# Optimization experiments

Hardware: AMD Instinct MI355X
Metric: run time of the kernel (lower is better)

## Reference

```python
import jax, jax.numpy as jnp
import numpy as np

# dims: T timesteps, B batch, IN input, OUT output, H controller hidden,
# N mem slots, C mem cell size, R read heads
T, B, IN, OUT, H, N, C, R = 512, 64, 256, 256, 512, 2048, 64, 4
EPS = 1e-8


def setup_inputs() -> dict:
    key = jax.random.key(0)
    ks = jax.random.split(key, 12)
    s = 0.02
    d_in = IN + C * R  # controller sees x_t concat flattened read vectors
    return {
        "xs": jax.random.normal(ks[0], (T, B, IN), jnp.float32),
        "W_ih": jax.random.normal(ks[1], (d_in, 4 * H), jnp.float32) * s,
        "W_hh": jax.random.normal(ks[2], (H, 4 * H), jnp.float32) * s,
        "b_lstm": jnp.zeros((4 * H,), jnp.float32),
        "W_out": jax.random.normal(ks[3], (H, OUT), jnp.float32) * s,
        "b_out": jnp.zeros((OUT,), jnp.float32),
        "W_key": jax.random.normal(ks[4], (H, C), jnp.float32) * s,
        "b_key": jnp.zeros((C,), jnp.float32),
        "W_beta": jax.random.normal(ks[5], (H, 1), jnp.float32) * s,
        "b_beta": jnp.zeros((1,), jnp.float32),
        "W_gen": jax.random.normal(ks[6], (H, C), jnp.float32) * s,
        "b_gen": jnp.zeros((C,), jnp.float32),
    }


def reference(xs, W_ih, W_hh, b_lstm, W_out, b_out, W_key, b_key,
              W_beta, b_beta, W_gen, b_gen):
    Bx = xs.shape[1]
    mem0 = jnp.zeros((Bx, N, C), xs.dtype)
    h0 = jnp.zeros((Bx, H), xs.dtype)
    c0 = jnp.zeros((Bx, H), xs.dtype)
    rv0 = jnp.zeros((Bx, C, R), xs.dtype)
    sl0 = jnp.zeros((), xs.dtype)

    def step(carry, x_t):
        h, c, mem, rv, sl = carry
        inp = jnp.concatenate([x_t, rv.reshape(Bx, -1)], axis=-1)
        gates = inp @ W_ih + h @ W_hh + b_lstm
        i_g, f_g, g_g, o_g = jnp.split(gates, 4, axis=-1)
        c = jax.nn.sigmoid(f_g) * c + jax.nn.sigmoid(i_g) * jnp.tanh(g_g)
        h = jax.nn.sigmoid(o_g) * jnp.tanh(c)
        pre_out = h @ W_out + b_out                    # (B, OUT)
        key = h @ W_key + b_key                        # (B, C)
        beta = jax.nn.softplus(h @ W_beta + b_beta)    # (B, 1)
        gen = h @ W_gen + b_gen                        # (B, C)
        # cosine similarity between each memory slot and the key
        num = jnp.einsum('bnc,bc->bn', mem, key)
        den = (jnp.maximum(jnp.linalg.norm(mem, axis=-1), EPS)
               * jnp.maximum(jnp.linalg.norm(key, axis=-1, keepdims=True), EPS))
        sim = num / den                                # (B, N)
        w = jax.nn.softmax(beta * sim, axis=-1)        # (B, N)
        # supervised (teacher) loss for this step
        sl = sl + jnp.mean((key - gen) ** 2)
        # additive content write: rank-1 update
        mem = mem + w[:, :, None] * key[:, None, :]
        # read: weights are the write weights repeated over read heads,
        # so all heads read the same vector -> compute once and broadcast
        r = jnp.einsum('bn,bnc->bc', w, mem)           # (B, C)
        rv = jnp.broadcast_to(r[:, :, None], (Bx, C, R))
        return (h, c, mem, rv, sl), pre_out

    (h, c, mem, rv, sup_loss), y_all = jax.lax.scan(
        step, (h0, c0, mem0, rv0, sl0), xs)
    return y_all, sup_loss
```

## Files before the change

kernel.cpp:

```cpp
#include <hip/hip_runtime.h>
#include <hip/hip_fp16.h>

#define EPSF 1e-8f
#define SCOPE_AGT __HIP_MEMORY_SCOPE_AGENT


typedef _Float16 h2_t __attribute__((ext_vector_type(2)));

struct P4 {
  const unsigned* W2h;
  const _Float16* Wkg;
  const _Float16* Wy;
  const float* b_lstm;
  const float* b_out;
  const float* b_key;
  const float* W_beta;
  const float* b_beta;
  const float* b_gen;
  const float* xs;
  float* hbuf;
  float* keyP;
  float* genP;
  float* yP;
  float* betaP;
  float* AccP;
  float* ZP;
  float* S2P;
  unsigned* ctr;
  float* out;
};

__device__ __forceinline__ float sigm(float x) { return 1.f / (1.f + __expf(-x)); }
__device__ __forceinline__ float aload(const float* p) {
  return __hip_atomic_load(p, __ATOMIC_RELAXED, SCOPE_AGT);
}
__device__ __forceinline__ void astore(float* p, float v) {
  __hip_atomic_store(p, v, __ATOMIC_RELAXED, SCOPE_AGT);
}

__global__ void __launch_bounds__(1024, 4) dnc_b4(P4 P) {
  const int tid   = threadIdx.x;
  const int bid   = blockIdx.x;
  const int chunk = (bid >> 1) & 3;
  const int b     = ((bid >> 3) << 1) | (bid & 1);
  const int lane  = tid & 63;
  const int wv    = tid >> 6;
  const int sgrp  = lane >> 4;
  const int c4    = lane & 15;

  __shared__ float s_inp[832];
  __shared__ float s_gates[512];
  __shared__ float s_c[128];
  __shared__ float s_part[4096];
  __shared__ float s_e[512];
  __shared__ float s_key[64], s_kprev[64], s_genv[64];
  __shared__ float s_wred[32];
  __shared__ float s_scal[4];

  unsigned* ctr = P.ctr + b * 32;

  float4 mreg[8];
  float  sden[8];
#pragma unroll
  for (int i = 0; i < 8; ++i) mreg[i] = make_float4(0.f, 0.f, 0.f, 0.f);

  for (int i = 256 + tid; i < 832; i += 1024) s_inp[i] = 0.f;
  if (tid < 128) s_c[tid] = 0.f;
  if (tid < 512) s_e[tid] = 0.f;
  if (tid < 64)  s_kprev[tid] = 0.f;
  float lossacc = 0.f;
  __syncthreads();

  const int q  = tid >> 7;
  const int cg = tid & 127;
  const unsigned* wbase = P.W2h + (size_t)chunk * 212992 + (cg << 2);

  for (int t = 0; t < 512; ++t) {
    if (tid < 128)
      ((float2*)s_inp)[tid] = ((const float2*)P.xs)[((size_t)t * 64 + b) * 128 + tid];
    __syncthreads();

    float4 acc = make_float4(0.f, 0.f, 0.f, 0.f);
    {
      const unsigned* wp = wbase + (size_t)(q * 48) * 512;
      const float* ip = s_inp + q * 96;
#pragma unroll 4
      for (int r = 0; r < 48; ++r) {
        const uint4 w = *(const uint4*)(wp + (size_t)r * 512);
        const float2 v = *(const float2*)(ip + r * 2);
        const __half2* h2 = (const __half2*)&w;
        const float2 f0 = __half22float2(h2[0]), f1 = __half22float2(h2[1]);
        const float2 f2 = __half22float2(h2[2]), f3 = __half22float2(h2[3]);
        acc.x = fmaf(v.x, f0.x, fmaf(v.y, f0.y, acc.x));
        acc.y = fmaf(v.x, f1.x, fmaf(v.y, f1.y, acc.y));
        acc.z = fmaf(v.x, f2.x, fmaf(v.y, f2.y, acc.z));
        acc.w = fmaf(v.x, f3.x, fmaf(v.y, f3.y, acc.w));
      }
    }

    if (t > 0) {
      if (tid == 0) {
        while (__hip_atomic_load(ctr, __ATOMIC_RELAXED, SCOPE_AGT) < 8u * (unsigned)t)
          __builtin_amdgcn_s_sleep(1);
      }
      __syncthreads();
      float a0 = 0.f, a1 = 0.f, a2 = 0.f, a3 = 0.f;
      if (tid < 64) {
        const float* ap = P.AccP + b * 256 + tid;
        a0 = aload(ap); a1 = aload(ap + 64); a2 = aload(ap + 128); a3 = aload(ap + 192);
      } else if (tid == 64) {
        const float* zp = P.ZP + b * 4;
        const float* sp = P.S2P + b * 4;
        const float Z  = aload(zp) + aload(zp + 1) + aload(zp + 2) + aload(zp + 3);
        const float S2 = aload(sp) + aload(sp + 1) + aload(sp + 2) + aload(sp + 3);
        s_scal[0] = 1.f / Z;  s_scal[1] = S2;
      }
      __syncthreads();
      if (tid < 64) {
        const float iZ = s_scal[0];
        s_inp[768 + tid] = iZ * ((a0 + a1 + a2 + a3) + s_scal[1] * iZ * s_kprev[tid]);
      }
      __syncthreads();
    } else {
      if (tid == 64) { s_scal[0] = 0.f; s_scal[1] = 0.f; }
      __syncthreads();
    }

    {
      const unsigned* wp = wbase + (size_t)(384 + q * 4) * 512;
      const float* ip = s_inp + 768 + q * 8;
#pragma unroll
      for (int r = 0; r < 4; ++r) {
        const uint4 w = *(const uint4*)(wp + (size_t)r * 512);
        const float2 v = *(const float2*)(ip + r * 2);
        const __half2* h2 = (const __half2*)&w;
        const float2 f0 = __half22float2(h2[0]), f1 = __half22float2(h2[1]);
        const float2 f2 = __half22float2(h2[2]), f3 = __half22float2(h2[3]);
        acc.x = fmaf(v.x, f0.x, fmaf(v.y, f0.y, acc.x));
        acc.y = fmaf(v.x, f1.x, fmaf(v.y, f1.y, acc.y));
        acc.z = fmaf(v.x, f2.x, fmaf(v.y, f2.y, acc.z));
        acc.w = fmaf(v.x, f3.x, fmaf(v.y, f3.y, acc.w));
      }
    }
    *(float4*)&s_part[(q << 9) + (cg << 2)] = acc;
    __syncthreads();

    if (tid < 512) {
      s_gates[tid] = s_part[tid]        + s_part[512 + tid]  + s_part[1024 + tid] + s_part[1536 + tid]
                   + s_part[2048 + tid] + s_part[2560 + tid] + s_part[3072 + tid] + s_part[3584 + tid];
    }
    __syncthreads();
    if (tid < 128) {
      const int jl = tid, cb = chunk * 128 + jl;
      const float gi = s_gates[jl * 4 + 0] + P.b_lstm[cb];
      const float gf = s_gates[jl * 4 + 1] + P.b_lstm[512 + cb];
      const float gg = s_gates[jl * 4 + 2] + P.b_lstm[1024 + cb];
      const float go = s_gates[jl * 4 + 3] + P.b_lstm[1536 + cb];
      const float cn = sigm(gf) * s_c[jl] + sigm(gi) * tanhf(gg);
      s_c[jl] = cn;
      const float hn = sigm(go) * tanhf(cn);
      s_inp[256 + cb] = hn;
      astore(P.hbuf + b * 512 + cb, hn);
    }
    __syncthreads();

    {
      const float* h = s_inp + 256 + chunk * 128;
      {
        const int isg = tid >> 9, rg = (tid >> 6) & 7, c = tid & 63;
        const _Float16* wp2 = P.Wkg + (size_t)(chunk * 128 + rg * 16) * 128 + isg * 64 + c;
        const float* hh = h + rg * 16;
        float a2 = 0.f;
#pragma unroll
        for (int r2 = 0; r2 < 16; ++r2) a2 = fmaf(hh[r2], (float)wp2[(size_t)r2 * 128], a2);
        s_part[tid] = a2;
      }
      {
        const int rg = tid >> 8, col = tid & 255;
        const _Float16* wp2 = P.Wy + (size_t)(chunk * 128 + rg * 32) * 256 + col;
        const float* hh = h + rg * 32;
        float a2 = 0.f;
#pragma unroll 8
        for (int r2 = 0; r2 < 32; ++r2) a2 = fmaf(hh[r2], (float)wp2[(size_t)r2 * 256], a2);
        s_part[1024 + (rg << 8) + col] = a2;
      }
      {
        float pb = (tid < 128) ? h[tid] * P.W_beta[chunk * 128 + tid] : 0.f;
#pragma unroll
        for (int off = 32; off; off >>= 1) pb += __shfl_down(pb, off);
        if (tid < 128 && lane == 0) s_wred[wv] = pb;
      }
    }
    __syncthreads();
    if (tid < 64) {
      float v = 0.f;
#pragma unroll
      for (int k = 0; k < 8; ++k) v += s_part[k * 64 + tid];
      astore(P.keyP + (b * 4 + chunk) * 64 + tid, v);
    } else if (tid < 128) {
      const int c = tid - 64;
      float v = 0.f;
#pragma unroll
      for (int k = 0; k < 8; ++k) v += s_part[512 + k * 64 + c];
      astore(P.genP + (b * 4 + chunk) * 64 + c, v);
    } else if (tid < 384) {
      const int col = tid - 128;
      astore(P.yP + (b * 4 + chunk) * 256 + col,
             s_part[1024 + col] + s_part[1280 + col] + s_part[1536 + col] + s_part[1792 + col]);
    } else if (tid == 384) {
      astore(P.betaP + b * 4 + chunk, s_wred[0] + s_wred[1]);
    }
    __syncthreads();
    if (tid == 0) __hip_atomic_fetch_add(ctr, 1u, __ATOMIC_RELEASE, SCOPE_AGT);

    {
      const float invZp = s_scal[0];
      const float4 kp4 = ((const float4*)s_kprev)[c4];
      const int nbase = (wv * 4 + sgrp) * 8;
#pragma unroll
      for (int it = 0; it < 8; ++it) {
        float4 m4 = mreg[it];
        const float wpv = s_e[nbase + it] * invZp;
        m4.x = fmaf(wpv, kp4.x, m4.x); m4.y = fmaf(wpv, kp4.y, m4.y);
        m4.z = fmaf(wpv, kp4.z, m4.z); m4.w = fmaf(wpv, kp4.w, m4.w);
        float ssq = m4.x * m4.x + m4.y * m4.y + m4.z * m4.z + m4.w * m4.w;
#pragma unroll
        for (int off = 1; off < 16; off <<= 1) ssq += __shfl_xor(ssq, off);
        sden[it] = fmaxf(sqrtf(ssq), EPSF);
        mreg[it] = m4;
      }
    }

    if (tid == 0) {
      while (__hip_atomic_load(ctr, __ATOMIC_RELAXED, SCOPE_AGT) < 8u * (unsigned)t + 4u)
        __builtin_amdgcn_s_sleep(1);
    }
    __syncthreads();
    if (tid < 64) {
      const float* kp = P.keyP + b * 256 + tid;
      s_key[tid] = aload(kp) + aload(kp + 64) + aload(kp + 128) + aload(kp + 192) + P.b_key[tid];
    } else if (tid < 128) {
      const int c = tid - 64;
      const float* gp = P.genP + b * 256 + c;
      s_genv[c] = aload(gp) + aload(gp + 64) + aload(gp + 128) + aload(gp + 192) + P.b_gen[c];
    } else if (tid < 192) {
      const int col = tid - 128, oc = chunk * 64 + col;
      const float* yp = P.yP + b * 1024 + oc;
      P.out[((size_t)t * 64 + b) * 256 + oc] =
          aload(yp) + aload(yp + 256) + aload(yp + 512) + aload(yp + 768) + P.b_out[oc];
    } else if (tid == 192) {
      const float* bp = P.betaP + b * 4;
      const float s = aload(bp) + aload(bp + 1) + aload(bp + 2) + aload(bp + 3) + P.b_beta[0];
      s_scal[2] = (s > 20.f) ? s : log1pf(__expf(s));
    } else if (tid >= 256 && tid < 640) {
      const int i = tid - 256;
      const int pc = i >> 7;
      const int pcc = pc + (pc >= chunk ? 1 : 0);
      const int jl = i & 127;
      s_inp[256 + pcc * 128 + jl] = aload(P.hbuf + b * 512 + pcc * 128 + jl);
    }
    __syncthreads();
    if (wv == 0) {
      const float kv = s_key[lane];
      float sq = kv * kv;
#pragma unroll
      for (int off = 32; off; off >>= 1) sq += __shfl_down(sq, off);
      if (lane == 0) s_scal[3] = fmaxf(sqrtf(sq), EPSF);
    } else if (wv == 1 && chunk == 0) {
      const float d = s_key[lane] - s_genv[lane];
      float ds = d * d;
#pragma unroll
      for (int off = 32; off; off >>= 1) ds += __shfl_down(ds, off);
      if (lane == 0) lossacc += ds;
    }
    __syncthreads();

    {
      const float beta = s_scal[2], kn = s_scal[3];
      const float4 kk = ((const float4*)s_key)[c4];
      float Zp = 0.f, S2p = 0.f;
      float4 acc4 = make_float4(0.f, 0.f, 0.f, 0.f);
      const int nbase = (wv * 4 + sgrp) * 8;
#pragma unroll
      for (int it = 0; it < 8; ++it) {
        const float4 m4 = mreg[it];
        float num = m4.x * kk.x + m4.y * kk.y + m4.z * kk.z + m4.w * kk.w;
#pragma unroll
        for (int off = 1; off < 16; off <<= 1) num += __shfl_xor(num, off);
        const float e = __expf(beta * (num / (sden[it] * kn)));
        if (c4 == 0) { s_e[nbase + it] = e; Zp += e; S2p += e * e; }
        acc4.x = fmaf(e, m4.x, acc4.x); acc4.y = fmaf(e, m4.y, acc4.y);
        acc4.z = fmaf(e, m4.z, acc4.z); acc4.w = fmaf(e, m4.w, acc4.w);
      }
#pragma unroll
      for (int off = 32; off; off >>= 1) { Zp += __shfl_down(Zp, off); S2p += __shfl_down(S2p, off); }
      if (lane == 0) { s_wred[wv] = Zp; s_wred[16 + wv] = S2p; }
#pragma unroll
      for (int off = 16; off < 64; off <<= 1) {
        acc4.x += __shfl_down(acc4.x, off); acc4.y += __shfl_down(acc4.y, off);
        acc4.z += __shfl_down(acc4.z, off); acc4.w += __shfl_down(acc4.w, off);
      }
      if (lane < 16) ((float4*)s_part)[wv * 16 + lane] = acc4;
    }
    __syncthreads();
    if (tid < 64) {
      float a = 0.f;
#pragma unroll
      for (int w = 0; w < 16; ++w) a += s_part[w * 64 + tid];
      astore(P.AccP + (b * 4 + chunk) * 64 + tid, a);
      s_kprev[tid] = s_key[tid];
    } else if (tid == 64) {
      float Z = 0.f, S2 = 0.f;
#pragma unroll
      for (int k = 0; k < 16; ++k) { Z += s_wred[k]; S2 += s_wred[16 + k]; }
      astore(P.ZP + b * 4 + chunk, Z);
      astore(P.S2P + b * 4 + chunk, S2);
    }
    __syncthreads();
    if (tid == 0) __hip_atomic_fetch_add(ctr, 1u, __ATOMIC_RELEASE, SCOPE_AGT);
  }

  if (chunk == 0 && tid == 64) atomicAdd(P.out + 8388608, lossacc * (1.f / 4096.f));
}

__global__ void build_w2h(const float* __restrict__ W_ih, const float* __restrict__ W_hh,
                          unsigned* __restrict__ W2h) {
  const int id = blockIdx.x * 256 + threadIdx.x;
  if (id >= 851968) return;
  const int chunk = id / 212992;
  const int rem   = id % 212992;
  const int rp    = rem >> 9;
  const int cc    = rem & 511;
  const int jl = cc >> 2, g = cc & 3;
  const int col = g * 512 + chunk * 128 + jl;
  float v[2];
#pragma unroll
  for (int k = 0; k < 2; ++k) {
    const int row = rp * 2 + k;
    if (row < 256)      v[k] = W_ih[(size_t)row * 2048 + col];
    else if (row < 768) v[k] = W_hh[(size_t)(row - 256) * 2048 + col];
    else {
      const float* p0 = W_ih + (size_t)(256 + (row - 768) * 4) * 2048 + col;
      v[k] = p0[0] + p0[2048] + p0[4096] + p0[6144];
    }
  }
  const __half2 h2v = __floats2half2_rn(v[0], v[1]);
  W2h[id] = *(const unsigned*)&h2v;
}

__global__ void build_wkg(const float* __restrict__ W_key, const float* __restrict__ W_gen,
                          _Float16* __restrict__ Wkg) {
  const int id = blockIdx.x * 256 + threadIdx.x;
  if (id >= 65536) return;
  const int row = id >> 7, cl = id & 127;
  const float v = (cl < 64) ? W_key[(size_t)row * 64 + cl] : W_gen[(size_t)row * 64 + cl - 64];
  Wkg[id] = (_Float16)v;
}

__global__ void build_wy(const float* __restrict__ W_out, _Float16* __restrict__ Wy) {
  const int id = blockIdx.x * 256 + threadIdx.x;
  if (id >= 131072) return;
  Wy[id] = (_Float16)W_out[id];
}

extern "C" void kernel_launch(void* const* d_in, const int* in_sizes, int n_in,
                              void* d_out, int out_size, void* d_ws, size_t ws_size,
                              hipStream_t stream) {
  const float* xs     = (const float*)d_in[0];
  const float* W_ih   = (const float*)d_in[1];
  const float* W_hh   = (const float*)d_in[2];
  const float* b_lstm = (const float*)d_in[3];
  const float* W_out  = (const float*)d_in[4];
  const float* b_out  = (const float*)d_in[5];
  const float* W_key  = (const float*)d_in[6];
  const float* b_key  = (const float*)d_in[7];
  const float* W_beta = (const float*)d_in[8];
  const float* b_beta = (const float*)d_in[9];
  const float* W_gen  = (const float*)d_in[10];
  const float* b_gen  = (const float*)d_in[11];
  float* out = (float*)d_out;

  float* ws = (float*)d_ws;
  unsigned* W2h = (unsigned*)ws;
  _Float16* Wkg = (_Float16*)(ws + 851968);
  _Float16* Wy  = (_Float16*)(ws + 884736);
  float* hbuf  = ws     + 950272;
  float* keyP  = hbuf   + 32768;
  float* genP  = keyP   + 16384;
  float* yP    = genP   + 16384;
  float* betaP = yP     + 65536;
  float* AccP  = betaP  + 256;
  float* ZP    = AccP   + 16384;
  float* S2P   = ZP     + 256;
  unsigned* ctr = (unsigned*)(S2P + 256);

  hipMemsetAsync(ctr, 0, 2048 * sizeof(unsigned), stream);
  hipMemsetAsync(out + 8388608, 0, sizeof(float), stream);

  build_w2h<<<dim3(3328), dim3(256), 0, stream>>>(W_ih, W_hh, W2h);
  build_wkg<<<dim3(256), dim3(256), 0, stream>>>(W_key, W_gen, Wkg);
  build_wy<<<dim3(512),  dim3(256), 0, stream>>>(W_out, Wy);

  P4 prm;
  prm.W2h = W2h; prm.Wkg = Wkg; prm.Wy = Wy;
  prm.b_lstm = b_lstm; prm.b_out = b_out; prm.b_key = b_key;
  prm.W_beta = W_beta; prm.b_beta = b_beta; prm.b_gen = b_gen;
  prm.xs = xs;
  prm.hbuf = hbuf; prm.keyP = keyP; prm.genP = genP; prm.yP = yP; prm.betaP = betaP;
  prm.AccP = AccP; prm.ZP = ZP; prm.S2P = S2P;
  prm.ctr = ctr;  prm.out = out;

  void* kargs[] = { &prm };
  hipLaunchCooperativeKernel(reinterpret_cast<void*>(&dnc_b4),
                             dim3(256), dim3(1024), kargs, 0, stream);
}
```

Before: 13.21 ms.

## Process two batch rows per block and use packed fp16 dot2 for matvecs

Each block now handles two batch elements instead of one, halving the grid to 128 blocks, so every weight load from the fp16 LSTM, key/gen and output matrices is reused for two rows. The matvec inputs are stored as fp16 in shared memory and accumulated with the fdot2 builtin on pair-packed weight layouts, and the key/gen/output weights are repacked as half2 pairs. Memory state for both rows is kept in registers, which doubles register and shared-memory pressure per block and halves parallelism across the device. Feeding h, x and the read vector as fp16 also lowers input precision.

Measured after the change: 25.31 ms. 91.7% more time.

```diff
diff --git a/kernel.cpp b/kernel.cpp
--- a/kernel.cpp
+++ b/kernel.cpp
@@ -7,10 +7,10 @@
 
 typedef _Float16 h2_t __attribute__((ext_vector_type(2)));
 
-struct P4 {
+struct P11 {
   const unsigned* W2h;
-  const _Float16* Wkg;
-  const _Float16* Wy;
+  const unsigned* Wkg2;
+  const unsigned* Wy2;
   const float* b_lstm;
   const float* b_out;
   const float* b_key;
@@ -37,37 +37,58 @@
 __device__ __forceinline__ void astore(float* p, float v) {
   __hip_atomic_store(p, v, __ATOMIC_RELAXED, SCOPE_AGT);
 }
-
-__global__ void __launch_bounds__(1024, 4) dnc_b4(P4 P) {
+__device__ __forceinline__ h2_t u2h(unsigned u) {
+  union { unsigned u; h2_t h; } x; x.u = u; return x.h;
+}
+
+#if defined(__has_builtin)
+#if __has_builtin(__builtin_amdgcn_fdot2)
+#define HAVE_FDOT2 1
+#endif
+#endif
+
+__device__ __forceinline__ float dot2acc(h2_t a, h2_t b, float c) {
+#ifdef HAVE_FDOT2
+  return __builtin_amdgcn_fdot2(a, b, c, false);
+#else
+  return fmaf((float)a.x, (float)b.x, fmaf((float)a.y, (float)b.y, c));
+#endif
+}
+
+__global__ void __launch_bounds__(1024, 4) dnc_b11(P11 P) {
   const int tid   = threadIdx.x;
   const int bid   = blockIdx.x;
   const int chunk = (bid >> 1) & 3;
-  const int b     = ((bid >> 3) << 1) | (bid & 1);
+  const int bp    = ((bid >> 3) << 1) | (bid & 1);
+  const int b0    = bp * 2;
   const int lane  = tid & 63;
   const int wv    = tid >> 6;
   const int sgrp  = lane >> 4;
   const int c4    = lane & 15;
 
-  __shared__ float s_inp[832];
-  __shared__ float s_gates[512];
-  __shared__ float s_c[128];
-  __shared__ float s_part[4096];
-  __shared__ float s_e[512];
-  __shared__ float s_key[64], s_kprev[64], s_genv[64];
-  __shared__ float s_wred[32];
-  __shared__ float s_scal[4];
-
-  unsigned* ctr = P.ctr + b * 32;
-
-  float4 mreg[8];
-  float  sden[8];
-#pragma unroll
-  for (int i = 0; i < 8; ++i) mreg[i] = make_float4(0.f, 0.f, 0.f, 0.f);
-
-  for (int i = 256 + tid; i < 832; i += 1024) s_inp[i] = 0.f;
-  if (tid < 128) s_c[tid] = 0.f;
-  if (tid < 512) s_e[tid] = 0.f;
-  if (tid < 64)  s_kprev[tid] = 0.f;
+  __shared__ _Float16 s_ih[2][832];
+  __shared__ float s_gates[2][512];
+  __shared__ float s_c[2][128];
+  __shared__ float s_part[8192];
+  __shared__ float s_e[2][512];
+  __shared__ float s_den[2][512];
+  __shared__ float s_key[2][64], s_kprev[2][64], s_genv[2][64];
+  __shared__ float s_wrZA[16], s_wrSA[16], s_wrZB[16], s_wrSB[16];
+  __shared__ float s_bred[2][2];
+  __shared__ float s_scal[2][4];
+
+  unsigned* ctr = P.ctr + bp * 32;
+
+  float4 mreg[2][8];
+#pragma unroll
+  for (int bb = 0; bb < 2; ++bb)
+#pragma unroll
+    for (int i = 0; i < 8; ++i) mreg[bb][i] = make_float4(0.f, 0.f, 0.f, 0.f);
+
+  for (int i = tid; i < 2 * 832; i += 1024) ((_Float16*)s_ih)[i] = (_Float16)0.f;
+  if (tid < 512) { s_e[0][tid] = 0.f; s_e[1][tid] = 0.f; }
+  if (tid < 128) { s_c[0][tid] = 0.f; s_c[1][tid] = 0.f; s_kprev[tid >> 6][tid & 63] = 0.f; }
+  if (tid < 8) s_scal[tid >> 2][tid & 3] = 0.f;
   float lossacc = 0.f;
   __syncthreads();
 
@@ -76,25 +97,29 @@
   const unsigned* wbase = P.W2h + (size_t)chunk * 212992 + (cg << 2);
 
   for (int t = 0; t < 512; ++t) {
-    if (tid < 128)
-      ((float2*)s_inp)[tid] = ((const float2*)P.xs)[((size_t)t * 64 + b) * 128 + tid];
-    __syncthreads();
-
-    float4 acc = make_float4(0.f, 0.f, 0.f, 0.f);
+    if (tid < 256) {
+      const int bb = tid >> 7, i = tid & 127;
+      const float2 xv = ((const float2*)P.xs)[((size_t)t * 64 + b0 + bb) * 128 + i];
+      h2_t hv; hv.x = (_Float16)xv.x; hv.y = (_Float16)xv.y;
+      *(h2_t*)&s_ih[bb][i * 2] = hv;
+    }
+    __syncthreads();
+
+    float4 accA = make_float4(0.f, 0.f, 0.f, 0.f);
+    float4 accB = make_float4(0.f, 0.f, 0.f, 0.f);
     {
       const unsigned* wp = wbase + (size_t)(q * 48) * 512;
-      const float* ip = s_inp + q * 96;
+      const _Float16* iA = &s_ih[0][q * 96];
+      const _Float16* iB = &s_ih[1][q * 96];
 #pragma unroll 4
       for (int r = 0; r < 48; ++r) {
         const uint4 w = *(const uint4*)(wp + (size_t)r * 512);
-        const float2 v = *(const float2*)(ip + r * 2);
-        const __half2* h2 = (const __half2*)&w;
-        const float2 f0 = __half22float2(h2[0]), f1 = __half22float2(h2[1]);
-        const float2 f2 = __half22float2(h2[2]), f3 = __half22float2(h2[3]);
-        acc.x = fmaf(v.x, f0.x, fmaf(v.y, f0.y, acc.x));
-        acc.y = fmaf(v.x, f1.x, fmaf(v.y, f1.y, acc.y));
-        acc.z = fmaf(v.x, f2.x, fmaf(v.y, f2.y, acc.z));
-        acc.w = fmaf(v.x, f3.x, fmaf(v.y, f3.y, acc.w));
+        const h2_t vA = *(const h2_t*)(iA + r * 2);
+        const h2_t vB = *(const h2_t*)(iB + r * 2);
+        accA.x = dot2acc(u2h(w.x), vA, accA.x); accB.x = dot2acc(u2h(w.x), vB, accB.x);
+        accA.y = dot2acc(u2h(w.y), vA, accA.y); accB.y = dot2acc(u2h(w.y), vB, accB.y);
+        accA.z = dot2acc(u2h(w.z), vA, accA.z); accB.z = dot2acc(u2h(w.z), vB, accB.z);
+        accA.w = dot2acc(u2h(w.w), vA, accA.w); accB.w = dot2acc(u2h(w.w), vB, accB.w);
       }
     }
 
@@ -105,129 +130,156 @@
       }
       __syncthreads();
       float a0 = 0.f, a1 = 0.f, a2 = 0.f, a3 = 0.f;
-      if (tid < 64) {
-        const float* ap = P.AccP + b * 256 + tid;
+      if (tid < 128) {
+        const int bb = tid >> 6, c = tid & 63;
+        const float* ap = P.AccP + (b0 + bb) * 256 + c;
         a0 = aload(ap); a1 = aload(ap + 64); a2 = aload(ap + 128); a3 = aload(ap + 192);
-      } else if (tid == 64) {
-        const float* zp = P.ZP + b * 4;
-        const float* sp = P.S2P + b * 4;
+      } else if (tid < 130) {
+        const int bb = tid - 128;
+        const float* zp = P.ZP + (b0 + bb) * 4;
+        const float* sp = P.S2P + (b0 + bb) * 4;
         const float Z  = aload(zp) + aload(zp + 1) + aload(zp + 2) + aload(zp + 3);
         const float S2 = aload(sp) + aload(sp + 1) + aload(sp + 2) + aload(sp + 3);
-        s_scal[0] = 1.f / Z;  s_scal[1] = S2;
+        s_scal[bb][0] = 1.f / Z;  s_scal[bb][1] = S2;
       }
       __syncthreads();
-      if (tid < 64) {
-        const float iZ = s_scal[0];
-        s_inp[768 + tid] = iZ * ((a0 + a1 + a2 + a3) + s_scal[1] * iZ * s_kprev[tid]);
+      if (tid < 128) {
+        const int bb = tid >> 6, c = tid & 63;
+        const float iZ = s_scal[bb][0];
+        const float r = iZ * ((a0 + a1 + a2 + a3) + s_scal[bb][1] * iZ * s_kprev[bb][c]);
+        s_ih[bb][768 + c] = (_Float16)r;
       }
       __syncthreads();
     } else {
-      if (tid == 64) { s_scal[0] = 0.f; s_scal[1] = 0.f; }
       __syncthreads();
     }
 
     {
       const unsigned* wp = wbase + (size_t)(384 + q * 4) * 512;
-      const float* ip = s_inp + 768 + q * 8;
+      const _Float16* iA = &s_ih[0][768 + q * 8];
+      const _Float16* iB = &s_ih[1][768 + q * 8];
 #pragma unroll
       for (int r = 0; r < 4; ++r) {
         const uint4 w = *(const uint4*)(wp + (size_t)r * 512);
-        const float2 v = *(const float2*)(ip + r * 2);
-        const __half2* h2 = (const __half2*)&w;
-        const float2 f0 = __half22float2(h2[0]), f1 = __half22float2(h2[1]);
-        const float2 f2 = __half22float2(h2[2]), f3 = __half22float2(h2[3]);
-        acc.x = fmaf(v.x, f0.x, fmaf(v.y, f0.y, acc.x));
-        acc.y = fmaf(v.x, f1.x, fmaf(v.y, f1.y, acc.y));
-        acc.z = fmaf(v.x, f2.x, fmaf(v.y, f2.y, acc.z));
-        acc.w = fmaf(v.x, f3.x, fmaf(v.y, f3.y, acc.w));
-      }
-    }
-    *(float4*)&s_part[(q << 9) + (cg << 2)] = acc;
-    __syncthreads();
-
-    if (tid < 512) {
-      s_gates[tid] = s_part[tid]        + s_part[512 + tid]  + s_part[1024 + tid] + s_part[1536 + tid]
-                   + s_part[2048 + tid] + s_part[2560 + tid] + s_part[3072 + tid] + s_part[3584 + tid];
-    }
-    __syncthreads();
-    if (tid < 128) {
-      const int jl = tid, cb = chunk * 128 + jl;
-      const float gi = s_gates[jl * 4 + 0] + P.b_lstm[cb];
-      const float gf = s_gates[jl * 4 + 1] + P.b_lstm[512 + cb];
-      const float gg = s_gates[jl * 4 + 2] + P.b_lstm[1024 + cb];
-      const float go = s_gates[jl * 4 + 3] + P.b_lstm[1536 + cb];
-      const float cn = sigm(gf) * s_c[jl] + sigm(gi) * tanhf(gg);
-      s_c[jl] = cn;
+        const h2_t vA = *(const h2_t*)(iA + r * 2);
+        const h2_t vB = *(const h2_t*)(iB + r * 2);
+        accA.x = dot2acc(u2h(w.x), vA, accA.x); accB.x = dot2acc(u2h(w.x), vB, accB.x);
+        accA.y = dot2acc(u2h(w.y), vA, accA.y); accB.y = dot2acc(u2h(w.y), vB, accB.y);
+        accA.z = dot2acc(u2h(w.z), vA, accA.z); accB.z = dot2acc(u2h(w.z), vB, accB.z);
+        accA.w = dot2acc(u2h(w.w), vA, accA.w); accB.w = dot2acc(u2h(w.w), vB, accB.w);
+      }
+    }
+    *(float4*)&s_part[(q << 9) + (cg << 2)]        = accA;
+    *(float4*)&s_part[4096 + (q << 9) + (cg << 2)] = accB;
+    __syncthreads();
+
+    {
+      const int bb = tid >> 9, col = tid & 511, off = bb * 4096;
+      float g = 0.f;
+#pragma unroll
+      for (int k = 0; k < 8; ++k) g += s_part[off + (k << 9) + col];
+      s_gates[bb][col] = g;
+    }
+    __syncthreads();
+
+    if (tid < 256) {
+      const int bb = tid >> 7, jl = tid & 127, cb = chunk * 128 + jl;
+      const float gi = s_gates[bb][jl * 4 + 0] + P.b_lstm[cb];
+      const float gf = s_gates[bb][jl * 4 + 1] + P.b_lstm[512 + cb];
+      const float gg = s_gates[bb][jl * 4 + 2] + P.b_lstm[1024 + cb];
+      const float go = s_gates[bb][jl * 4 + 3] + P.b_lstm[1536 + cb];
+      const float cn = sigm(gf) * s_c[bb][jl] + sigm(gi) * tanhf(gg);
+      s_c[bb][jl] = cn;
       const float hn = sigm(go) * tanhf(cn);
-      s_inp[256 + cb] = hn;
-      astore(P.hbuf + b * 512 + cb, hn);
-    }
-    __syncthreads();
-
-    {
-      const float* h = s_inp + 256 + chunk * 128;
+      s_ih[bb][256 + cb] = (_Float16)hn;
+      astore(P.hbuf + (b0 + bb) * 512 + cb, hn);
+    }
+    __syncthreads();
+
+    {
       {
         const int isg = tid >> 9, rg = (tid >> 6) & 7, c = tid & 63;
-        const _Float16* wp2 = P.Wkg + (size_t)(chunk * 128 + rg * 16) * 128 + isg * 64 + c;
-        const float* hh = h + rg * 16;
-        float a2 = 0.f;
-#pragma unroll
-        for (int r2 = 0; r2 < 16; ++r2) a2 = fmaf(hh[r2], (float)wp2[(size_t)r2 * 128], a2);
-        s_part[tid] = a2;
+#pragma unroll
+        for (int bb = 0; bb < 2; ++bb) {
+          float a = 0.f;
+#pragma unroll
+          for (int k = 0; k < 8; ++k) {
+            const unsigned w = P.Wkg2[(size_t)(chunk * 64 + rg * 8 + k) * 128 + isg * 64 + c];
+            const h2_t v = *(const h2_t*)&s_ih[bb][256 + chunk * 128 + rg * 16 + 2 * k];
+            a = dot2acc(u2h(w), v, a);
+          }
+          s_part[bb * 2048 + rg * 128 + isg * 64 + c] = a;
+        }
       }
       {
         const int rg = tid >> 8, col = tid & 255;
-        const _Float16* wp2 = P.Wy + (size_t)(chunk * 128 + rg * 32) * 256 + col;
-        const float* hh = h + rg * 32;
-        float a2 = 0.f;
-#pragma unroll 8
-        for (int r2 = 0; r2 < 32; ++r2) a2 = fmaf(hh[r2], (float)wp2[(size_t)r2 * 256], a2);
-        s_part[1024 + (rg << 8) + col] = a2;
+#pragma unroll
+        for (int bb = 0; bb < 2; ++bb) {
+          float a = 0.f;
+#pragma unroll
+          for (int k = 0; k < 16; ++k) {
+            const unsigned w = P.Wy2[(size_t)(chunk * 64 + rg * 16 + k) * 256 + col];
+            const h2_t v = *(const h2_t*)&s_ih[bb][256 + chunk * 128 + rg * 32 + 2 * k];
+            a = dot2acc(u2h(w), v, a);
+          }
+          s_part[bb * 2048 + 1024 + (rg << 8) + col] = a;
+        }
       }
       {
-        float pb = (tid < 128) ? h[tid] * P.W_beta[chunk * 128 + tid] : 0.f;
-#pragma unroll
-        for (int off = 32; off; off >>= 1) pb += __shfl_down(pb, off);
-        if (tid < 128 && lane == 0) s_wred[wv] = pb;
-      }
-    }
-    __syncthreads();
-    if (tid < 64) {
-      float v = 0.f;
-#pragma unroll
-      for (int k = 0; k < 8; ++k) v += s_part[k * 64 + tid];
-      astore(P.keyP + (b * 4 + chunk) * 64 + tid, v);
-    } else if (tid < 128) {
-      const int c = tid - 64;
-      float v = 0.f;
-#pragma unroll
-      for (int k = 0; k < 8; ++k) v += s_part[512 + k * 64 + c];
-      astore(P.genP + (b * 4 + chunk) * 64 + c, v);
-    } else if (tid < 384) {
-      const int col = tid - 128;
-      astore(P.yP + (b * 4 + chunk) * 256 + col,
-             s_part[1024 + col] + s_part[1280 + col] + s_part[1536 + col] + s_part[1792 + col]);
-    } else if (tid == 384) {
-      astore(P.betaP + b * 4 + chunk, s_wred[0] + s_wred[1]);
+        if (tid < 128 || (tid >= 512 && tid < 640)) {
+          const int bb = tid >> 9, i = tid & 127;
+          const float hv = (float)s_ih[bb][256 + chunk * 128 + i];
+          float pb = hv * P.W_beta[chunk * 128 + i];
+#pragma unroll
+          for (int off = 32; off; off >>= 1) pb += __shfl_down(pb, off);
+          if (lane == 0) s_bred[bb][wv & 1] = pb;
+        }
+      }
+    }
+    __syncthreads();
+    {
+      const int bb = tid >> 9, t2 = tid & 511, off = bb * 2048;
+      if (t2 < 64) {
+        float v = 0.f;
+#pragma unroll
+        for (int k = 0; k < 8; ++k) v += s_part[off + k * 128 + t2];
+        astore(P.keyP + ((b0 + bb) * 4 + chunk) * 64 + t2, v);
+      } else if (t2 < 128) {
+        const int c = t2 - 64;
+        float v = 0.f;
+#pragma unroll
+        for (int k = 0; k < 8; ++k) v += s_part[off + k * 128 + 64 + c];
+        astore(P.genP + ((b0 + bb) * 4 + chunk) * 64 + c, v);
+      } else if (t2 < 384) {
+        const int col = t2 - 128;
+        astore(P.yP + ((b0 + bb) * 4 + chunk) * 256 + col,
+               s_part[off + 1024 + col] + s_part[off + 1280 + col]
+             + s_part[off + 1536 + col] + s_part[off + 1792 + col]);
+      } else if (t2 == 384) {
+        astore(P.betaP + (b0 + bb) * 4 + chunk, s_bred[bb][0] + s_bred[bb][1]);
+      }
     }
     __syncthreads();
     if (tid == 0) __hip_atomic_fetch_add(ctr, 1u, __ATOMIC_RELEASE, SCOPE_AGT);
 
     {
-      const float invZp = s_scal[0];
-      const float4 kp4 = ((const float4*)s_kprev)[c4];
       const int nbase = (wv * 4 + sgrp) * 8;
 #pragma unroll
-      for (int it = 0; it < 8; ++it) {
-        float4 m4 = mreg[it];
-        const float wpv = s_e[nbase + it] * invZp;
-        m4.x = fmaf(wpv, kp4.x, m4.x); m4.y = fmaf(wpv, kp4.y, m4.y);
-        m4.z = fmaf(wpv, kp4.z, m4.z); m4.w = fmaf(wpv, kp4.w, m4.w);
-        float ssq = m4.x * m4.x + m4.y * m4.y + m4.z * m4.z + m4.w * m4.w;
-#pragma unroll
-        for (int off = 1; off < 16; off <<= 1) ssq += __shfl_xor(ssq, off);
-        sden[it] = fmaxf(sqrtf(ssq), EPSF);
-        mreg[it] = m4;
+      for (int bb = 0; bb < 2; ++bb) {
+        const float invZp = s_scal[bb][0];
+        const float4 kp4 = ((const float4*)s_kprev[bb])[c4];
+#pragma unroll
+        for (int it = 0; it < 8; ++it) {
+          float4 m4 = mreg[bb][it];
+          const float wpv = s_e[bb][nbase + it] * invZp;
+          m4.x = fmaf(wpv, kp4.x, m4.x); m4.y = fmaf(wpv, kp4.y, m4.y);
+          m4.z = fmaf(wpv, kp4.z, m4.z); m4.w = fmaf(wpv, kp4.w, m4.w);
+          float ssq = m4.x * m4.x + m4.y * m4.y + m4.z * m4.z + m4.w * m4.w;
+#pragma unroll
+          for (int off = 1; off < 16; off <<= 1) ssq += __shfl_xor(ssq, off);
+          if (c4 == 0) s_den[bb][nbase + it] = fmaxf(sqrtf(ssq), EPSF);
+          mreg[bb][it] = m4;
+        }
       }
     }
 
@@ -236,38 +288,48 @@
         __builtin_amdgcn_s_sleep(1);
     }
     __syncthreads();
-    if (tid < 64) {
-      const float* kp = P.keyP + b * 256 + tid;
-      s_key[tid] = aload(kp) + aload(kp + 64) + aload(kp + 128) + aload(kp + 192) + P.b_key[tid];
-    } else if (tid < 128) {
-      const int c = tid - 64;
-      const float* gp = P.genP + b * 256 + c;
-      s_genv[c] = aload(gp) + aload(gp + 64) + aload(gp + 128) + aload(gp + 192) + P.b_gen[c];
-    } else if (tid < 192) {
-      const int col = tid - 128, oc = chunk * 64 + col;
-      const float* yp = P.yP + b * 1024 + oc;
-      P.out[((size_t)t * 64 + b) * 256 + oc] =
-          aload(yp) + aload(yp + 256) + aload(yp + 512) + aload(yp + 768) + P.b_out[oc];
-    } else if (tid == 192) {
-      const float* bp = P.betaP + b * 4;
-      const float s = aload(bp) + aload(bp + 1) + aload(bp + 2) + aload(bp + 3) + P.b_beta[0];
-      s_scal[2] = (s > 20.f) ? s : log1pf(__expf(s));
-    } else if (tid >= 256 && tid < 640) {
-      const int i = tid - 256;
+    if (tid < 768) {
+      const int bb = (tid >= 384) ? 1 : 0;
+      const int i = tid - bb * 384;
       const int pc = i >> 7;
       const int pcc = pc + (pc >= chunk ? 1 : 0);
       const int jl = i & 127;
-      s_inp[256 + pcc * 128 + jl] = aload(P.hbuf + b * 512 + pcc * 128 + jl);
-    }
-    __syncthreads();
-    if (wv == 0) {
-      const float kv = s_key[lane];
+      const float hv = aload(P.hbuf + (b0 + bb) * 512 + pcc * 128 + jl);
+      s_ih[bb][256 + pcc * 128 + jl] = (_Float16)hv;
+    }
+    {
+      const int bb = tid >> 8;
+      const int t2 = tid & 255;
+      if (tid < 512) {
+        if (t2 < 64) {
+          const float* kp = P.keyP + (b0 + bb) * 256 + t2;
+          s_key[bb][t2] = aload(kp) + aload(kp + 64) + aload(kp + 128) + aload(kp + 192) + P.b_key[t2];
+        } else if (t2 < 128) {
+          const int c = t2 - 64;
+          const float* gp = P.genP + (b0 + bb) * 256 + c;
+          s_genv[bb][c] = aload(gp) + aload(gp + 64) + aload(gp + 128) + aload(gp + 192) + P.b_gen[c];
+        } else if (t2 < 192) {
+          const int col = t2 - 128, oc = chunk * 64 + col;
+          const float* yp = P.yP + (b0 + bb) * 1024 + oc;
+          P.out[((size_t)t * 64 + b0 + bb) * 256 + oc] =
+              aload(yp) + aload(yp + 256) + aload(yp + 512) + aload(yp + 768) + P.b_out[oc];
+        } else if (t2 == 192) {
+          const float* bpt = P.betaP + (b0 + bb) * 4;
+          const float s = aload(bpt) + aload(bpt + 1) + aload(bpt + 2) + aload(bpt + 3) + P.b_beta[0];
+          s_scal[bb][2] = (s > 20.f) ? s : log1pf(__expf(s));
+        }
+      }
+    }
+    __syncthreads();
+    if (wv < 2) {
+      const float kv = s_key[wv][lane];
       float sq = kv * kv;
 #pragma unroll
       for (int off = 32; off; off >>= 1) sq += __shfl_down(sq, off);
-      if (lane == 0) s_scal[3] = fmaxf(sqrtf(sq), EPSF);
-    } else if (wv == 1 && chunk == 0) {
-      const float d = s_key[lane] - s_genv[lane];
+      if (lane == 0) s_scal[wv][3] = fmaxf(sqrtf(sq), EPSF);
+    } else if ((wv == 2 || wv == 3) && chunk == 0) {
+      const int bb = wv - 2;
+      const float d = s_key[bb][lane] - s_genv[bb][lane];
       float ds = d * d;
 #pragma unroll
       for (int off = 32; off; off >>= 1) ds += __shfl_down(ds, off);
@@ -276,51 +338,88 @@
     __syncthreads();
 
     {
-      const float beta = s_scal[2], kn = s_scal[3];
-      const float4 kk = ((const float4*)s_key)[c4];
-      float Zp = 0.f, S2p = 0.f;
-      float4 acc4 = make_float4(0.f, 0.f, 0.f, 0.f);
       const int nbase = (wv * 4 + sgrp) * 8;
+      const float betaA = s_scal[0][2], knA = s_scal[0][3];
+      const float betaB = s_scal[1][2], knB = s_scal[1][3];
+      const float4 kkA = ((const float4*)s_key[0])[c4];
+      const float4 kkB = ((const float4*)s_key[1])[c4];
+      float ZpA = 0.f, S2pA = 0.f, ZpB = 0.f, S2pB = 0.f;
+      float4 acA = make_float4(0.f, 0.f, 0.f, 0.f);
+      float4 acB = make_float4(0.f, 0.f, 0.f, 0.f);
 #pragma unroll
       for (int it = 0; it < 8; ++it) {
-        const float4 m4 = mreg[it];
-        float num = m4.x * kk.x + m4.y * kk.y + m4.z * kk.z + m4.w * kk.w;
-#pragma unroll
-        for (int off = 1; off < 16; off <<= 1) num += __shfl_xor(num, off);
-        const float e = __expf(beta * (num / (sden[it] * kn)));
-        if (c4 == 0) { s_e[nbase + it] = e; Zp += e; S2p += e * e; }
-        acc4.x = fmaf(e, m4.x, acc4.x); acc4.y = fmaf(e, m4.y, acc4.y);
-        acc4.z = fmaf(e, m4.z, acc4.z); acc4.w = fmaf(e, m4.w, acc4.w);
-      }
-#pragma unroll
-      for (int off = 32; off; off >>= 1) { Zp += __shfl_down(Zp, off); S2p += __shfl_down(S2p, off); }
-      if (lane == 0) { s_wred[wv] = Zp; s_wred[16 + wv] = S2p; }
+        {
+          const float4 m4 = mreg[0][it];
+          float num = m4.x * kkA.x + m4.y * kkA.y + m4.z * kkA.z + m4.w * kkA.w;
+#pragma unroll
+          for (int off = 1; off < 16; off <<= 1) num += __shfl_xor(num, off);
+          const float e = __expf(betaA * (num / (s_den[0][nbase + it] * knA)));
+          if (c4 == 0) { s_e[0][nbase + it] = e; ZpA += e; S2pA += e * e; }
+          acA.x = fmaf(e, m4.x, acA.x); acA.y = fmaf(e, m4.y, acA.y);
+          acA.z = fmaf(e, m4.z, acA.z); acA.w = fmaf(e, m4.w, acA.w);
+        }
+        {
+          const float4 m4 = mreg[1][it];
+          float num = m4.x * kkB.x + m4.y * kkB.y + m4.z * kkB.z + m4.w * kkB.w;
+#pragma unroll
+          for (int off = 1; off < 16; off <<= 1) num += __shfl_xor(num, off);
+          const float e = __expf(betaB * (num / (s_den[1][nbase + it] * knB)));
+          if (c4 == 0) { s_e[1][nbase + it] = e; ZpB += e; S2pB += e * e; }
+          acB.x = fmaf(e, m4.x, acB.x); acB.y = fmaf(e, m4.y, acB.y);
+          acB.z = fmaf(e, m4.z, acB.z); acB.w = fmaf(e, m4.w, acB.w);
+        }
+      }
+#pragma unroll
+      for (int off = 32; off; off >>= 1) {
+        ZpA += __shfl_down(ZpA, off); S2pA += __shfl_down(S2pA, off);
+        ZpB += __shfl_down(ZpB, off); S2pB += __shfl_down(S2pB, off);
+      }
+      if (lane == 0) { s_wrZA[wv] = ZpA; s_wrSA[wv] = S2pA; s_wrZB[wv] = ZpB; s_wrSB[wv] = S2pB; }
 #pragma unroll
       for (int off = 16; off < 64; off <<= 1) {
-        acc4.x += __shfl_down(acc4.x, off); acc4.y += __shfl_down(acc4.y, off);
-        acc4.z += __shfl_down(acc4.z, off); acc4.w += __shfl_down(acc4.w, off);
-      }
-      if (lane < 16) ((float4*)s_part)[wv * 16 + lane] = acc4;
+        acA.x += __shfl_down(acA.x, off); acA.y += __shfl_down(acA.y, off);
+        acA.z += __shfl_down(acA.z, off); acA.w += __shfl_down(acA.w, off);
+        acB.x += __shfl_down(acB.x, off); acB.y += __shfl_down(acB.y, off);
+        acB.z += __shfl_down(acB.z, off); acB.w += __shfl_down(acB.w, off);
+      }
+      if (lane < 16) {
+        ((float4*)s_part)[wv * 16 + lane]       = acA;
+        ((float4*)s_part)[256 + wv * 16 + lane] = acB;
+      }
     }
     __syncthreads();
     if (tid < 64) {
       float a = 0.f;
 #pragma unroll
       for (int w = 0; w < 16; ++w) a += s_part[w * 64 + tid];
-      astore(P.AccP + (b * 4 + chunk) * 64 + tid, a);
-      s_kprev[tid] = s_key[tid];
+      astore(P.AccP + (b0 * 4 + chunk) * 64 + tid, a);
+      s_kprev[0][tid] = s_key[0][tid];
     } else if (tid == 64) {
       float Z = 0.f, S2 = 0.f;
 #pragma unroll
-      for (int k = 0; k < 16; ++k) { Z += s_wred[k]; S2 += s_wred[16 + k]; }
-      astore(P.ZP + b * 4 + chunk, Z);
-      astore(P.S2P + b * 4 + chunk, S2);
+      for (int k = 0; k < 16; ++k) { Z += s_wrZA[k]; S2 += s_wrSA[k]; }
+      astore(P.ZP + b0 * 4 + chunk, Z);
+      astore(P.S2P + b0 * 4 + chunk, S2);
+    } else if (tid >= 128 && tid < 192) {
+      const int c = tid - 128;
+      float a = 0.f;
+#pragma unroll
+      for (int w = 0; w < 16; ++w) a += s_part[1024 + w * 64 + c];
+      astore(P.AccP + ((b0 + 1) * 4 + chunk) * 64 + c, a);
+      s_kprev[1][c] = s_key[1][c];
+    } else if (tid == 192) {
+      float Z = 0.f, S2 = 0.f;
+#pragma unroll
+      for (int k = 0; k < 16; ++k) { Z += s_wrZB[k]; S2 += s_wrSB[k]; }
+      astore(P.ZP + (b0 + 1) * 4 + chunk, Z);
+      astore(P.S2P + (b0 + 1) * 4 + chunk, S2);
     }
     __syncthreads();
     if (tid == 0) __hip_atomic_fetch_add(ctr, 1u, __ATOMIC_RELEASE, SCOPE_AGT);
   }
 
-  if (chunk == 0 && tid == 64) atomicAdd(P.out + 8388608, lossacc * (1.f / 4096.f));
+  if (chunk == 0 && (tid == 128 || tid == 192))
+    atomicAdd(P.out + 8388608, lossacc * (1.f / 4096.f));
 }
 
 __global__ void build_w2h(const float* __restrict__ W_ih, const float* __restrict__ W_hh,
@@ -348,19 +447,28 @@
   W2h[id] = *(const unsigned*)&h2v;
 }
 
-__global__ void build_wkg(const float* __restrict__ W_key, const float* __restrict__ W_gen,
-                          _Float16* __restrict__ Wkg) {
+__global__ void build_wkg2(const float* __restrict__ W_key, const float* __restrict__ W_gen,
+                           unsigned* __restrict__ Wkg2) {
+  const int id = blockIdx.x * 256 + threadIdx.x;
+  if (id >= 32768) return;
+  const int rp = id >> 7, cl = id & 127;
+  float v[2];
+#pragma unroll
+  for (int k = 0; k < 2; ++k) {
+    const int row = rp * 2 + k;
+    v[k] = (cl < 64) ? W_key[(size_t)row * 64 + cl] : W_gen[(size_t)row * 64 + cl - 64];
+  }
+  const __half2 h2v = __floats2half2_rn(v[0], v[1]);
+  Wkg2[id] = *(const unsigned*)&h2v;
+}
+
+__global__ void build_wy2(const float* __restrict__ W_out, unsigned* __restrict__ Wy2) {
   const int id = blockIdx.x * 256 + threadIdx.x;
   if (id >= 65536) return;
-  const int row = id >> 7, cl = id & 127;
-  const float v = (cl < 64) ? W_key[(size_t)row * 64 + cl] : W_gen[(size_t)row * 64 + cl - 64];
-  Wkg[id] = (_Float16)v;
-}
-
-__global__ void build_wy(const float* __restrict__ W_out, _Float16* __restrict__ Wy) {
-  const int id = blockIdx.x * 256 + threadIdx.x;
-  if (id >= 131072) return;
-  Wy[id] = (_Float16)W_out[id];
+  const int rp = id >> 8, col = id & 255;
+  const __half2 h2v = __floats2half2_rn(W_out[(size_t)(rp * 2) * 256 + col],
+                                        W_out[(size_t)(rp * 2 + 1) * 256 + col]);
+  Wy2[id] = *(const unsigned*)&h2v;
 }
 
 extern "C" void kernel_launch(void* const* d_in, const int* in_sizes, int n_in,
@@ -381,9 +489,9 @@
   float* out = (float*)d_out;
 
   float* ws = (float*)d_ws;
-  unsigned* W2h = (unsigned*)ws;
-  _Float16* Wkg = (_Float16*)(ws + 851968);
-  _Float16* Wy  = (_Float16*)(ws + 884736);
+  unsigned* W2h  = (unsigned*)ws;
+  unsigned* Wkg2 = (unsigned*)(ws + 851968);
+  unsigned* Wy2  = (unsigned*)(ws + 884736);
   float* hbuf  = ws     + 950272;
   float* keyP  = hbuf   + 32768;
   float* genP  = keyP   + 16384;
@@ -394,15 +502,15 @@
   float* S2P   = ZP     + 256;
   unsigned* ctr = (unsigned*)(S2P + 256);
 
-  hipMemsetAsync(ctr, 0, 2048 * sizeof(unsigned), stream);
+  hipMemsetAsync(ctr, 0, 1024 * sizeof(unsigned), stream);
   hipMemsetAsync(out + 8388608, 0, sizeof(float), stream);
 
   build_w2h<<<dim3(3328), dim3(256), 0, stream>>>(W_ih, W_hh, W2h);
-  build_wkg<<<dim3(256), dim3(256), 0, stream>>>(W_key, W_gen, Wkg);
-  build_wy<<<dim3(512),  dim3(256), 0, stream>>>(W_out, Wy);
-
-  P4 prm;
-  prm.W2h = W2h; prm.Wkg = Wkg; prm.Wy = Wy;
+  build_wkg2<<<dim3(128), dim3(256), 0, stream>>>(W_key, W_gen, Wkg2);
+  build_wy2<<<dim3(256),  dim3(256), 0, stream>>>(W_out, Wy2);
+
+  P11 prm;
+  prm.W2h = W2h; prm.Wkg2 = Wkg2; prm.Wy2 = Wy2;
   prm.b_lstm = b_lstm; prm.b_out = b_out; prm.b_key = b_key;
   prm.W_beta = W_beta; prm.b_beta = b_beta; prm.b_gen = b_gen;
   prm.xs = xs;
@@ -411,6 +519,6 @@
   prm.ctr = ctr;  prm.out = out;
 
   void* kargs[] = { &prm };
-  hipLaunchCooperativeKernel(reinterpret_cast<void*>(&dnc_b4),
-                             dim3(256), dim3(1024), kargs, 0, stream);
-}
+  hipLaunchCooperativeKernel(reinterpret_cast<void*>(&dnc_b11),
+                             dim3(128), dim3(1024), kargs, 0, stream);
+}
```
